# Kernel tuning notes

Measured on AMD Instinct MI355X. Metric: run time of the kernel, lower is better.

Reference implementation:

```python
import jax, jax.numpy as jnp
import numpy as np


def setup_inputs() -> dict:
    key = jax.random.key(0)
    k1, k2 = jax.random.split(key)
    x = jax.random.normal(k1, (16, 256, 128, 128), dtype=jnp.float32)
    conv_w = jax.random.normal(k2, (1, 2, 3, 3), dtype=jnp.float32) * 0.1
    return {"x": x, "conv_w": conv_w}


def reference(x, conv_w):
    # x: [B, C, H, W]; channel-wise mean and max -> [B, 2, H, W]
    x_avg = jnp.mean(x, axis=1, keepdims=True)
    x_max = jnp.max(x, axis=1, keepdims=True)
    feat = jnp.concatenate([x_avg, x_max], axis=1)
    # 3x3 conv, stride 1, padding 1, no bias; NCHW / OIHW
    y = jax.lax.conv_general_dilated(
        feat, conv_w,
        window_strides=(1, 1), padding=((1, 1), (1, 1)),
        dimension_numbers=("NCHW", "OIHW", "NCHW"))
    return jax.nn.sigmoid(y)  # [B, 1, H, W]
```

## Files before the change

kernel.cpp:

```cpp
#include <hip/hip_runtime.h>
#include <math.h>

#define B 16
#define C 256
#define H 128
#define W 128
#define HW (H * W)
#define HW4 (HW / 4)

typedef float vfloat4 __attribute__((ext_vector_type(4)));

__global__ __launch_bounds__(512) void reduce_mean_max(
    const float* __restrict__ x, float* __restrict__ feat) {
  const int t    = threadIdx.x;
  const int lane = t & 63;
  const int wv   = t >> 6;
  const int sp   = blockIdx.x;
  const int b    = sp >> 4;
  const int s4b  = (sp & 15) << 8;

  const vfloat4* xp =
      (const vfloat4*)x + (size_t)(b * C + wv * 32) * HW4 + s4b;

  vfloat4 sum[4], mx[4];
#pragma unroll
  for (int i = 0; i < 4; ++i) {
    sum[i] = (vfloat4)(0.f);
    mx[i]  = (vfloat4)(-INFINITY);
  }

#pragma unroll 4
  for (int c = 0; c < 32; ++c) {
    const vfloat4* p = xp + (size_t)c * HW4;
#pragma unroll
    for (int i = 0; i < 4; ++i) {
      vfloat4 v = p[i * 64 + lane];
      sum[i] += v;
      mx[i].x = fmaxf(mx[i].x, v.x);
      mx[i].y = fmaxf(mx[i].y, v.y);
      mx[i].z = fmaxf(mx[i].z, v.z);
      mx[i].w = fmaxf(mx[i].w, v.w);
    }
  }

  __shared__ vfloat4 s_buf[8][64][4];

#pragma unroll
  for (int i = 0; i < 4; ++i) s_buf[wv][lane][i] = sum[i];
  __syncthreads();
  if (t < 256) {
    const int i = t >> 6, l = t & 63;
    vfloat4 a = (vfloat4)(0.f);
#pragma unroll
    for (int w2 = 0; w2 < 8; ++w2) a += s_buf[w2][l][i];
    const float inv = 1.0f / (float)C;
    ((vfloat4*)feat)[(size_t)(b * 2) * HW4 + s4b + t] = a * inv;
  }
  __syncthreads();

#pragma unroll
  for (int i = 0; i < 4; ++i) s_buf[wv][lane][i] = mx[i];
  __syncthreads();
  if (t < 256) {
    const int i = t >> 6, l = t & 63;
    vfloat4 m = s_buf[0][l][i];
#pragma unroll
    for (int w2 = 1; w2 < 8; ++w2) {
      vfloat4 v = s_buf[w2][l][i];
      m.x = fmaxf(m.x, v.x);
      m.y = fmaxf(m.y, v.y);
      m.z = fmaxf(m.z, v.z);
      m.w = fmaxf(m.w, v.w);
    }
    ((vfloat4*)feat)[(size_t)(b * 2 + 1) * HW4 + s4b + t] = m;
  }
}

__global__ __launch_bounds__(256) void conv3x3_sigmoid(
    const float* __restrict__ feat, const float* __restrict__ wgt,
    float* __restrict__ out) {
  __shared__ float sw[18];
  if (threadIdx.x < 18) sw[threadIdx.x] = wgt[threadIdx.x];
  __syncthreads();

  const int idx = blockIdx.x * 256 + threadIdx.x;
  const int b = idx >> 14;
  const int s = idx & (HW - 1);
  const int h = s >> 7;
  const int w = s & (W - 1);

  float acc = 0.f;
#pragma unroll
  for (int ci = 0; ci < 2; ++ci) {
    const float* f  = feat + (size_t)(b * 2 + ci) * HW;
    const float* kw = sw + ci * 9;
#pragma unroll
    for (int dh = -1; dh <= 1; ++dh) {
      const int hh = h + dh;
      if (hh < 0 || hh >= H) continue;
      const float* row = f + hh * W;
#pragma unroll
      for (int dw = -1; dw <= 1; ++dw) {
        const int ww = w + dw;
        if (ww < 0 || ww >= W) continue;
        acc += row[ww] * kw[(dh + 1) * 3 + (dw + 1)];
      }
    }
  }
  out[idx] = 1.f / (1.f + __expf(-acc));
}

extern "C" void kernel_launch(void* const* d_in, const int* in_sizes, int n_in,
                              void* d_out, int out_size, void* d_ws, size_t ws_size,
                              hipStream_t stream) {
  const float* x   = (const float*)d_in[0];
  const float* wgt = (const float*)d_in[1];
  float* out  = (float*)d_out;
  float* feat = (float*)d_ws;

  reduce_mean_max<<<256, 512, 0, stream>>>(x, feat);
  conv3x3_sigmoid<<<1024, 256, 0, stream>>>(feat, wgt, out);
}
```

Measured before the change: 353.8 us.

## Fuse channel mean/max reduction with 3x3 conv and sigmoid into one kernel

Each block now reduces mean and max over channels for an 8-row strip plus one halo row on each side. It keeps the two feature maps in shared memory and applies the 3x3 convolution and sigmoid directly. This removes the intermediate workspace write and read and the second kernel launch. In exchange each block reads up to 25% more input rows for the halo, and each thread holds more accumulators.

```diff
diff --git a/kernel.cpp b/kernel.cpp
--- a/kernel.cpp
+++ b/kernel.cpp
@@ -7,24 +7,35 @@
 #define W 128
 #define HW (H * W)
 #define HW4 (HW / 4)
+#define W4 (W / 4)
 
 typedef float vfloat4 __attribute__((ext_vector_type(4)));
 
-__global__ __launch_bounds__(512) void reduce_mean_max(
-    const float* __restrict__ x, float* __restrict__ feat) {
+__global__ __launch_bounds__(512) void fused_mean_max_conv(
+    const float* __restrict__ x, const float* __restrict__ wgt,
+    float* __restrict__ out) {
   const int t    = threadIdx.x;
   const int lane = t & 63;
   const int wv   = t >> 6;
-  const int sp   = blockIdx.x;
-  const int b    = sp >> 4;
-  const int s4b  = (sp & 15) << 8;
+  const int b    = blockIdx.x >> 4;
+  const int r0   = (blockIdx.x & 15) << 3;
+  const int rlo  = (r0 == 0) ? 0 : r0 - 1;
+  const int rhi  = (r0 == 120) ? 127 : r0 + 8;
+  const int nchunks = (rhi - rlo + 1) * W4;
 
-  const vfloat4* xp =
-      (const vfloat4*)x + (size_t)(b * C + wv * 32) * HW4 + s4b;
+  __shared__ float   sw[18];
+  __shared__ vfloat4 s_buf[8][320];
+  __shared__ float   fmean[1280];
+  __shared__ float   fmaxv[1280];
 
-  vfloat4 sum[4], mx[4];
+  if (t < 18) sw[t] = wgt[t];
+
+  const vfloat4* xp = (const vfloat4*)x +
+      (size_t)(b * C + wv * 32) * HW4 + rlo * W4;
+
+  vfloat4 sum[5], mx[5];
 #pragma unroll
-  for (int i = 0; i < 4; ++i) {
+  for (int i = 0; i < 5; ++i) {
     sum[i] = (vfloat4)(0.f);
     mx[i]  = (vfloat4)(-INFINITY);
   }
@@ -33,81 +44,73 @@
   for (int c = 0; c < 32; ++c) {
     const vfloat4* p = xp + (size_t)c * HW4;
 #pragma unroll
-    for (int i = 0; i < 4; ++i) {
-      vfloat4 v = p[i * 64 + lane];
-      sum[i] += v;
-      mx[i].x = fmaxf(mx[i].x, v.x);
-      mx[i].y = fmaxf(mx[i].y, v.y);
-      mx[i].z = fmaxf(mx[i].z, v.z);
-      mx[i].w = fmaxf(mx[i].w, v.w);
+    for (int i = 0; i < 5; ++i) {
+      const int j = i * 64 + lane;
+      if (j < nchunks) {
+        vfloat4 v = p[j];
+        sum[i] += v;
+        mx[i].x = fmaxf(mx[i].x, v.x);
+        mx[i].y = fmaxf(mx[i].y, v.y);
+        mx[i].z = fmaxf(mx[i].z, v.z);
+        mx[i].w = fmaxf(mx[i].w, v.w);
+      }
     }
   }
 
-  __shared__ vfloat4 s_buf[8][64][4];
-
 #pragma unroll
-  for (int i = 0; i < 4; ++i) s_buf[wv][lane][i] = sum[i];
+  for (int i = 0; i < 5; ++i) s_buf[wv][i * 64 + lane] = sum[i];
   __syncthreads();
-  if (t < 256) {
-    const int i = t >> 6, l = t & 63;
+  if (t < nchunks) {
     vfloat4 a = (vfloat4)(0.f);
 #pragma unroll
-    for (int w2 = 0; w2 < 8; ++w2) a += s_buf[w2][l][i];
-    const float inv = 1.0f / (float)C;
-    ((vfloat4*)feat)[(size_t)(b * 2) * HW4 + s4b + t] = a * inv;
+    for (int w2 = 0; w2 < 8; ++w2) a += s_buf[w2][t];
+    ((vfloat4*)fmean)[t] = a * (1.0f / (float)C);
   }
   __syncthreads();
-
 #pragma unroll
-  for (int i = 0; i < 4; ++i) s_buf[wv][lane][i] = mx[i];
+  for (int i = 0; i < 5; ++i) s_buf[wv][i * 64 + lane] = mx[i];
   __syncthreads();
-  if (t < 256) {
-    const int i = t >> 6, l = t & 63;
-    vfloat4 m = s_buf[0][l][i];
+  if (t < nchunks) {
+    vfloat4 m = s_buf[0][t];
 #pragma unroll
     for (int w2 = 1; w2 < 8; ++w2) {
-      vfloat4 v = s_buf[w2][l][i];
+      vfloat4 v = s_buf[w2][t];
       m.x = fmaxf(m.x, v.x);
       m.y = fmaxf(m.y, v.y);
       m.z = fmaxf(m.z, v.z);
       m.w = fmaxf(m.w, v.w);
     }
-    ((vfloat4*)feat)[(size_t)(b * 2 + 1) * HW4 + s4b + t] = m;
+    ((vfloat4*)fmaxv)[t] = m;
   }
-}
-
-__global__ __launch_bounds__(256) void conv3x3_sigmoid(
-    const float* __restrict__ feat, const float* __restrict__ wgt,
-    float* __restrict__ out) {
-  __shared__ float sw[18];
-  if (threadIdx.x < 18) sw[threadIdx.x] = wgt[threadIdx.x];
   __syncthreads();
 
-  const int idx = blockIdx.x * 256 + threadIdx.x;
-  const int b = idx >> 14;
-  const int s = idx & (HW - 1);
-  const int h = s >> 7;
-  const int w = s & (W - 1);
+#pragma unroll
+  for (int oo = 0; oo < 2; ++oo) {
+    const int o  = t + oo * 512;
+    const int ro = o >> 7;
+    const int w  = o & (W - 1);
+    const int r  = r0 + ro;
 
-  float acc = 0.f;
+    float acc = 0.f;
 #pragma unroll
-  for (int ci = 0; ci < 2; ++ci) {
-    const float* f  = feat + (size_t)(b * 2 + ci) * HW;
-    const float* kw = sw + ci * 9;
+    for (int ci = 0; ci < 2; ++ci) {
+      const float* f  = ci ? fmaxv : fmean;
+      const float* kw = sw + ci * 9;
 #pragma unroll
-    for (int dh = -1; dh <= 1; ++dh) {
-      const int hh = h + dh;
-      if (hh < 0 || hh >= H) continue;
-      const float* row = f + hh * W;
+      for (int dh = -1; dh <= 1; ++dh) {
+        const int rr = r + dh;
+        if (rr < 0 || rr >= H) continue;
+        const float* frow = f + (rr - rlo) * W;
 #pragma unroll
-      for (int dw = -1; dw <= 1; ++dw) {
-        const int ww = w + dw;
-        if (ww < 0 || ww >= W) continue;
-        acc += row[ww] * kw[(dh + 1) * 3 + (dw + 1)];
+        for (int dw = -1; dw <= 1; ++dw) {
+          const int ww = w + dw;
+          if (ww < 0 || ww >= W) continue;
+          acc += frow[ww] * kw[(dh + 1) * 3 + (dw + 1)];
+        }
       }
     }
+    out[(size_t)b * HW + r0 * W + o] = 1.f / (1.f + __expf(-acc));
   }
-  out[idx] = 1.f / (1.f + __expf(-acc));
 }
 
 extern "C" void kernel_launch(void* const* d_in, const int* in_sizes, int n_in,
@@ -115,9 +118,8 @@
                               hipStream_t stream) {
   const float* x   = (const float*)d_in[0];
   const float* wgt = (const float*)d_in[1];
-  float* out  = (float*)d_out;
-  float* feat = (float*)d_ws;
+  float* out = (float*)d_out;
+  (void)d_ws; (void)ws_size;
 
-  reduce_mean_max<<<256, 512, 0, stream>>>(x, feat);
-  conv3x3_sigmoid<<<1024, 256, 0, stream>>>(feat, wgt, out);
+  fused_mean_max_conv<<<256, 512, 0, stream>>>(x, wgt, out);
 }
```

New measurement: 385.5 us. +9.0%, slower.
